# Kernel optimization log

Measured on AMD Instinct MI355X. Metric: run time of the kernel, lower is better.

Reference implementation:

```python
import jax, jax.numpy as jnp
import numpy as np

D_MODEL = 1024
NUM_HEADS = 16
DEPTH = D_MODEL // NUM_HEADS
NEG_INF = -1e9


def setup_inputs() -> dict:
    key = jax.random.key(0)
    ks = jax.random.split(key, 12)
    B, S = 4, 2048
    scale = 1.0 / np.sqrt(D_MODEL)
    inp = {
        "q": jax.random.normal(ks[0], (B, S, D_MODEL), jnp.float32),
        "k": jax.random.normal(ks[1], (B, S, D_MODEL), jnp.float32),
        "v": jax.random.normal(ks[2], (B, S, D_MODEL), jnp.float32),
        "mask": jax.random.randint(ks[3], (B, 1, 1, S), 0, 2, jnp.int32),
        "wq": jax.random.normal(ks[4], (D_MODEL, D_MODEL), jnp.float32) * scale,
        "bq": jnp.zeros((D_MODEL,), jnp.float32),
        "wk": jax.random.normal(ks[5], (D_MODEL, D_MODEL), jnp.float32) * scale,
        "bk": jnp.zeros((D_MODEL,), jnp.float32),
        "wv": jax.random.normal(ks[6], (D_MODEL, D_MODEL), jnp.float32) * scale,
        "bv": jnp.zeros((D_MODEL,), jnp.float32),
        "wo": jax.random.normal(ks[7], (D_MODEL, D_MODEL), jnp.float32) * scale,
        "bo": jnp.zeros((D_MODEL,), jnp.float32),
    }
    return inp


def _split_heads(x):
    # [B, S, D] -> [B, H, S, depth]
    B, S, _ = x.shape
    return x.reshape(B, S, NUM_HEADS, DEPTH).transpose(0, 2, 1, 3)


def reference(q, k, v, mask, wq, bq, wk, bk, wv, bv, wo, bo):
    B, S, _ = q.shape
    qh = _split_heads(q @ wq + bq)  # [B,H,S,d]
    kh = _split_heads(k @ wk + bk)
    vh = _split_heads(v @ wv + bv)
    logits = jnp.einsum("bhqd,bhkd->bhqk", qh, kh) / jnp.sqrt(
        jnp.asarray(DEPTH, jnp.float32))
    logits = logits + mask.astype(jnp.float32) * NEG_INF
    weights = jax.nn.softmax(logits, axis=-1)
    attn = jnp.einsum("bhqk,bhkd->bhqd", weights, vh)
    attn = attn.transpose(0, 2, 1, 3).reshape(B, S, D_MODEL)
    return attn @ wo + bo
```

## Files before the change

### kernel.cpp

```cpp
#include <hip/hip_runtime.h>

#define SB 4
#define SS 2048
#define SD 1024
#define SH 16

typedef float f32x4 __attribute__((ext_vector_type(4)));
typedef __bf16 bf16x8 __attribute__((ext_vector_type(8)));
typedef short short4v __attribute__((ext_vector_type(4)));
typedef unsigned int uint2v __attribute__((ext_vector_type(2)));

__device__ __forceinline__ unsigned short f2bf_(float x) {
    unsigned u = __builtin_bit_cast(unsigned, x);
    unsigned r = u + 0x7FFFu + ((u >> 16) & 1u);
    return (unsigned short)(r >> 16);
}

#define GL2LDS(g, l) __builtin_amdgcn_global_load_lds( \
    (const __attribute__((address_space(1))) unsigned int*)(g), \
    (__attribute__((address_space(3))) unsigned int*)(l), 16, 0, 0)

__global__ __launch_bounds__(256) void maskprep(
        const int* __restrict__ mk, float* __restrict__ MA, int n) {
    int i = blockIdx.x * 256 + threadIdx.x;
    if (i < n)
        MA[i] = (float)mk[i] * (-1e9f * 1.4426950408889634f) - 8.0f;
}

__global__ __launch_bounds__(256) void transpose4(
        const float* __restrict__ w0, const float* __restrict__ w1,
        const float* __restrict__ w2, const float* __restrict__ w3,
        unsigned short* __restrict__ out) {
    __shared__ unsigned short tile[32][33];
    int zz = blockIdx.z;
    const float* src = (zz == 0) ? w0 : (zz == 1) ? w1 : (zz == 2) ? w2 : w3;
    unsigned short* dst = out + (size_t)zz * 1024 * 1024;
    int x = blockIdx.x * 32 + threadIdx.x;
    int y0 = blockIdx.y * 32;
    for (int j = threadIdx.y; j < 32; j += 8)
        tile[j][threadIdx.x] = f2bf_(src[(size_t)(y0 + j) * 1024 + x]);
    __syncthreads();
    int ox = y0 + threadIdx.x;
    int oy0 = blockIdx.x * 32;
    for (int j = threadIdx.y; j < 32; j += 8)
        dst[(size_t)(oy0 + j) * 1024 + ox] = tile[threadIdx.x][j];
}

template <int STORE_MODE>
__global__ __launch_bounds__(256) void gemm_proj(
        const float* __restrict__ Af, const unsigned short* __restrict__ BT,
        const float* __restrict__ bias, unsigned short* __restrict__ C,
        float oscale) {
    const int K = 1024, N = 1024;
    __shared__ alignas(16) float Asmf[2][128][32];
    __shared__ alignas(16) unsigned short Bsm[2][128][32];
    const int m0 = blockIdx.x * 128, n0 = blockIdx.y * 128;
    const int lane = threadIdx.x & 63, wid = threadIdx.x >> 6;
    const int wr = wid >> 1, wc = wid & 1;
    const int cl = lane & 15, kg = lane >> 4;

    f32x4 acc[4][4] = {};

    auto STAGE = [&](int buf, int k0) {
#pragma unroll
        for (int i = 0; i < 4; ++i) {
            int base = i * 32 + wid * 8;
            int row = base + (lane >> 3);
            int cs = (lane & 7) ^ (row & 7);
            GL2LDS(Af + (size_t)(m0 + row) * K + k0 + cs * 4, &Asmf[buf][base][0]);
        }
#pragma unroll
        for (int i = 0; i < 2; ++i) {
            int base = (i * 4 + wid) * 16;
            int row = base + (lane >> 2);
            int cs = (lane & 3) ^ ((row >> 1) & 3);
            GL2LDS(BT + (size_t)(n0 + row) * K + k0 + cs * 8, &Bsm[buf][base][0]);
        }
    };

    STAGE(0, 0);
    __syncthreads();

    for (int k0 = 0; k0 < K; k0 += 32) {
        int cur = (k0 >> 5) & 1;
        if (k0 + 32 < K) STAGE(cur ^ 1, k0 + 32);

        bf16x8 af[4], bfv[4];
#pragma unroll
        for (int mi = 0; mi < 4; ++mi) {
            int r = wr * 64 + mi * 16 + cl;
            const float* Ar = &Asmf[cur][r][0];
            f32x4 a0 = *(const f32x4*)(Ar + ((2 * kg) ^ (r & 7)) * 4);
            f32x4 a1 = *(const f32x4*)(Ar + ((2 * kg + 1) ^ (r & 7)) * 4);
#pragma unroll
            for (int e = 0; e < 4; ++e) {
                af[mi][e] = (__bf16)a0[e];
                af[mi][4 + e] = (__bf16)a1[e];
            }
        }
#pragma unroll
        for (int ni = 0; ni < 4; ++ni) {
            int r = wc * 64 + ni * 16 + cl;
            bfv[ni] = *(const bf16x8*)&Bsm[cur][r][(kg ^ ((r >> 1) & 3)) * 8];
        }
#pragma unroll
        for (int mi = 0; mi < 4; ++mi)
#pragma unroll
            for (int ni = 0; ni < 4; ++ni)
                acc[mi][ni] = __builtin_amdgcn_mfma_f32_16x16x32_bf16(
                    af[mi], bfv[ni], acc[mi][ni], 0, 0, 0);
        __syncthreads();
    }

    const int rl = (lane >> 4) * 4;
#pragma unroll
    for (int mi = 0; mi < 4; ++mi) {
#pragma unroll
        for (int ni = 0; ni < 4; ++ni) {
            int row = m0 + wr * 64 + mi * 16 + rl;
            int col = n0 + wc * 64 + ni * 16 + cl;
            float bv = bias[col];
            f32x4 v = acc[mi][ni];
            if (STORE_MODE == 0) {
#pragma unroll
                for (int j = 0; j < 4; ++j)
                    C[(size_t)(row + j) * N + col] = f2bf_((v[j] + bv) * oscale);
            } else {
                int bb = row >> 11, s = row & 2047;
                short4v pk;
#pragma unroll
                for (int j = 0; j < 4; ++j)
                    pk[j] = (short)f2bf_(v[j] + bv);
                *(short4v*)&C[((size_t)(bb * 1024 + col)) * 2048 + s] = pk;
            }
        }
    }
}

__global__ __launch_bounds__(256) void gemm_out(
        const unsigned short* __restrict__ Ab, const unsigned short* __restrict__ BT,
        const float* __restrict__ bias, float* __restrict__ C,
        int M, int N, int K) {
    __shared__ alignas(16) unsigned short Asmb[2][128][32];
    __shared__ alignas(16) unsigned short Bsm[2][128][32];
    const int m0 = blockIdx.x * 128, n0 = blockIdx.y * 128;
    const int lane = threadIdx.x & 63, wid = threadIdx.x >> 6;
    const int wr = wid >> 1, wc = wid & 1;
    const int cl = lane & 15, kg = lane >> 4;

    f32x4 acc[4][4] = {};

    auto STAGE = [&](int buf, int k0) {
#pragma unroll
        for (int i = 0; i < 2; ++i) {
            int base = (i * 4 + wid) * 16;
            int row = base + (lane >> 2);
            int cs = (lane & 3) ^ ((row >> 1) & 3);
            GL2LDS(Ab + (size_t)(m0 + row) * K + k0 + cs * 8, &Asmb[buf][base][0]);
            GL2LDS(BT + (size_t)(n0 + row) * K + k0 + cs * 8, &Bsm[buf][base][0]);
        }
    };

    STAGE(0, 0);
    __syncthreads();

    for (int k0 = 0; k0 < K; k0 += 32) {
        int cur = (k0 >> 5) & 1;
        if (k0 + 32 < K) STAGE(cur ^ 1, k0 + 32);

        bf16x8 af[4], bfv[4];
#pragma unroll
        for (int mi = 0; mi < 4; ++mi) {
            int r = wr * 64 + mi * 16 + cl;
            af[mi] = *(const bf16x8*)&Asmb[cur][r][(kg ^ ((r >> 1) & 3)) * 8];
        }
#pragma unroll
        for (int ni = 0; ni < 4; ++ni) {
            int r = wc * 64 + ni * 16 + cl;
            bfv[ni] = *(const bf16x8*)&Bsm[cur][r][(kg ^ ((r >> 1) & 3)) * 8];
        }
#pragma unroll
        for (int mi = 0; mi < 4; ++mi)
#pragma unroll
            for (int ni = 0; ni < 4; ++ni)
                acc[mi][ni] = __builtin_amdgcn_mfma_f32_16x16x32_bf16(
                    af[mi], bfv[ni], acc[mi][ni], 0, 0, 0);
        __syncthreads();
    }

    const int rl = (lane >> 4) * 4;
#pragma unroll
    for (int mi = 0; mi < 4; ++mi) {
#pragma unroll
        for (int ni = 0; ni < 4; ++ni) {
            int row = m0 + wr * 64 + mi * 16 + rl;
            int col = n0 + wc * 64 + ni * 16 + cl;
            float bv = bias[col];
            f32x4 v = acc[mi][ni];
#pragma unroll
            for (int j = 0; j < 4; ++j)
                C[(size_t)(row + j) * N + col] = v[j] + bv;
        }
    }
}

__global__ __launch_bounds__(512, 4) void attn_kernel(
        const unsigned short* __restrict__ Qp, const unsigned short* __restrict__ Kp,
        const unsigned short* __restrict__ VT, const float* __restrict__ MA,
        unsigned short* __restrict__ O) {
    __shared__ alignas(16) unsigned short Klds[2][128][64];
    __shared__ alignas(16) unsigned short Vlds[2][64][128];
    const int lane = threadIdx.x & 63, wid = threadIdx.x >> 6;
    const int bh = blockIdx.x;
    const int b = bh >> 4, h = bh & 15;
    const int qt = blockIdx.y;
    const int qrow0 = qt * 256 + wid * 32;
    const int cl = lane & 15, kg = lane >> 4;

    bf16x8 qf[2][2];
#pragma unroll
    for (int qh = 0; qh < 2; ++qh)
#pragma unroll
        for (int kh = 0; kh < 2; ++kh)
            qf[qh][kh] = *(const bf16x8*)&Qp[(size_t)(b * SS + qrow0 + qh * 16 + cl) * SD
                                            + h * 64 + kh * 32 + kg * 8];

    const float* MAb = MA + b * SS;

    f32x4 oacc[2][4] = {};
    f32x4 lsum[2] = {};

    auto STAGE = [&](int buf, int tt) {
        int kt = (tt & 15) * 128;
        {
            int r8 = lane >> 3, c8 = lane & 7;
#pragma unroll
            for (int i = 0; i < 2; ++i) {
                int r = i * 64 + wid * 8 + r8;
                int cs = c8 ^ (r & 7);
                GL2LDS(Kp + (size_t)(b * SS + kt + r) * SD + h * 64 + cs * 8,
                       &Klds[buf][i * 64 + wid * 8][0]);
            }
        }
        {
            int r16 = lane >> 4, c16 = lane & 15;
#pragma unroll
            for (int i = 0; i < 2; ++i) {
                int r = i * 32 + wid * 4 + r16;
                int cs = (c16 & 8) | ((c16 & 7) ^ (r & 7));
                GL2LDS(VT + (size_t)(b * 1024 + h * 64 + r) * 2048 + kt + cs * 8,
                       &Vlds[buf][i * 32 + wid * 4][0]);
            }
        }
    };

    auto QKCOL = [&](int buf, int kt, int cf, f32x4* sv) {
        int r = cf * 16 + cl;
        bf16x8 kf0 = *(const bf16x8*)&Klds[buf][r][((0 + kg) ^ (r & 7)) * 8];
        bf16x8 kf1 = *(const bf16x8*)&Klds[buf][r][((4 + kg) ^ (r & 7)) * 8];
        f32x4 M = *(const f32x4*)&MAb[kt + cf * 16 + 4 * kg];
        __builtin_amdgcn_s_setprio(1);
#pragma unroll
        for (int qh = 0; qh < 2; ++qh) {
            f32x4 s = {};
            s = __builtin_amdgcn_mfma_f32_16x16x32_bf16(kf0, qf[qh][0], s, 0, 0, 0);
            s = __builtin_amdgcn_mfma_f32_16x16x32_bf16(kf1, qf[qh][1], s, 0, 0, 0);
#pragma unroll
            for (int j = 0; j < 4; ++j)
                s[j] = __builtin_amdgcn_exp2f(s[j] + M[j]);
            sv[qh] = s;
            lsum[qh] += s;
        }
        __builtin_amdgcn_s_setprio(0);
    };

    auto STEP = [&](int buf, int t) {
        int kt = t * 128;
#pragma unroll
        for (int ks = 0; ks < 4; ++ks) {
            f32x4 sA[2], sB[2];
            QKCOL(buf, kt, ks, sA);
            QKCOL(buf, kt, ks + 4, sB);
            bf16x8 pa[2];
#pragma unroll
            for (int qh = 0; qh < 2; ++qh) {
                pa[qh][0] = (__bf16)sA[qh][0];
                pa[qh][1] = (__bf16)sA[qh][1];
                pa[qh][2] = (__bf16)sA[qh][2];
                pa[qh][3] = (__bf16)sA[qh][3];
                pa[qh][4] = (__bf16)sB[qh][0];
                pa[qh][5] = (__bf16)sB[qh][1];
                pa[qh][6] = (__bf16)sB[qh][2];
                pa[qh][7] = (__bf16)sB[qh][3];
            }
            __builtin_amdgcn_s_setprio(1);
#pragma unroll
            for (int nf = 0; nf < 4; ++nf) {
                int d = nf * 16 + cl;
                int c16a = 2 * ks + (kg >> 1);
                int c16b = 2 * (ks + 4) + (kg >> 1);
                int cha = (c16a & 8) | ((c16a & 7) ^ (d & 7));
                int chb = (c16b & 8) | ((c16b & 7) ^ (d & 7));
                const char* vb = (const char*)&Vlds[buf][d][0];
                uint2v lo = *(const uint2v*)(vb + cha * 16 + (kg & 1) * 8);
                uint2v hi = *(const uint2v*)(vb + chb * 16 + (kg & 1) * 8);
                bf16x8 vf;
                *(uint2v*)&vf = lo;
                *((uint2v*)&vf + 1) = hi;
#pragma unroll
                for (int qh = 0; qh < 2; ++qh)
                    oacc[qh][nf] = __builtin_amdgcn_mfma_f32_16x16x32_bf16(
                        pa[qh], vf, oacc[qh][nf], 0, 0, 0);
            }
            __builtin_amdgcn_s_setprio(0);
        }
    };

    STAGE(0, 0);
    __syncthreads();
    for (int t = 0; t < 16; ++t) {
        int cur = t & 1;
        STAGE(cur ^ 1, t + 1);
        STEP(cur, t);
        __syncthreads();
    }

    float lfull[2];
#pragma unroll
    for (int qh = 0; qh < 2; ++qh) {
        float l = (lsum[qh][0] + lsum[qh][1]) + (lsum[qh][2] + lsum[qh][3]);
        l += __shfl_xor(l, 16);
        l += __shfl_xor(l, 32);
        lfull[qh] = l;
    }
#pragma unroll
    for (int qh = 0; qh < 2; ++qh) {
#pragma unroll
        for (int j = 0; j < 4; ++j) {
            float inv = 1.0f / __shfl(lfull[qh], 4 * kg + j);
#pragma unroll
            for (int nf = 0; nf < 4; ++nf)
                O[(size_t)(b * SS + qrow0 + qh * 16 + 4 * kg + j) * SD + h * 64 + nf * 16 + cl] =
                    f2bf_(oacc[qh][nf][j] * inv);
        }
    }
}

extern "C" void kernel_launch(void* const* d_in, const int* in_sizes, int n_in,
                              void* d_out, int out_size, void* d_ws, size_t ws_size,
                              hipStream_t stream) {
    const float* q  = (const float*)d_in[0];
    const float* k  = (const float*)d_in[1];
    const float* v  = (const float*)d_in[2];
    const int*   mk = (const int*)d_in[3];
    const float* wq = (const float*)d_in[4];
    const float* bq = (const float*)d_in[5];
    const float* wk = (const float*)d_in[6];
    const float* bk = (const float*)d_in[7];
    const float* wv = (const float*)d_in[8];
    const float* bv = (const float*)d_in[9];
    const float* wo = (const float*)d_in[10];
    const float* bo = (const float*)d_in[11];
    float* out = (float*)d_out;

    char* ws = (char*)d_ws;
    unsigned short* WT  = (unsigned short*)ws;
    unsigned short* X   = (unsigned short*)(ws + 8388608);
    unsigned short* Qh  = (unsigned short*)(ws + 25165824);
    unsigned short* Kh  = (unsigned short*)(ws + 41943040);
    unsigned short* VTr = (unsigned short*)(ws + 58720256);
    float*          MAf = (float*)(ws + 75497472);

    const float QSCL = 0.125f * 1.4426950408889634f;

    transpose4<<<dim3(32, 32, 4), dim3(32, 8), 0, stream>>>(wq, wk, wv, wo, WT);
    maskprep<<<dim3(32), dim3(256), 0, stream>>>(mk, MAf, SB * SS);

    dim3 gg(64, 8), gb(256);

    gemm_proj<0><<<gg, gb, 0, stream>>>(q, WT,               bq, Qh,  QSCL);
    gemm_proj<0><<<gg, gb, 0, stream>>>(k, WT + 1048576,     bk, Kh,  1.0f);
    gemm_proj<1><<<gg, gb, 0, stream>>>(v, WT + 2 * 1048576, bv, VTr, 1.0f);

    attn_kernel<<<dim3(64, 8), dim3(512), 0, stream>>>(Qh, Kh, VTr, MAf, X);

    gemm_out<<<dim3(64, 8), dim3(256), 0, stream>>>(
        X, WT + 3 * 1048576, bo, out, 8192, 1024, 1024);
}
```

Measured before the change: 213.7 us.

## Merge QKV projection launches and compute softmax row sums via MFMA

The three Q/K/V projection GEMM launches become one launch with a z-dimension that selects the input, weights, bias and store layout per block. This removes launch gaps and gives a larger grid of 1536 blocks for the GPU to fill. In the attention kernel, the per-lane VALU accumulation of exp values plus the final cross-lane shuffle reduction is replaced by an extra MFMA per step that multiplies the bf16 probabilities by a ones vector. That saves VALU adds and shuffles but adds matrix-core work, and the row sums now come from bf16-rounded probabilities, which keeps them consistent with the values used in P·V.

```diff
diff --git a/kernel.cpp b/kernel.cpp
--- a/kernel.cpp
+++ b/kernel.cpp
@@ -46,14 +46,21 @@
         dst[(size_t)(oy0 + j) * 1024 + ox] = tile[threadIdx.x][j];
 }
 
-template <int STORE_MODE>
-__global__ __launch_bounds__(256) void gemm_proj(
-        const float* __restrict__ Af, const unsigned short* __restrict__ BT,
-        const float* __restrict__ bias, unsigned short* __restrict__ C,
-        float oscale) {
+__global__ __launch_bounds__(256) void gemm_qkv(
+        const float* __restrict__ Aq, const float* __restrict__ Ak,
+        const float* __restrict__ Avv, const unsigned short* __restrict__ WT,
+        const float* __restrict__ bq, const float* __restrict__ bk,
+        const float* __restrict__ bv, unsigned short* __restrict__ Qh,
+        unsigned short* __restrict__ Kh, unsigned short* __restrict__ VTr,
+        float qscl) {
     const int K = 1024, N = 1024;
     __shared__ alignas(16) float Asmf[2][128][32];
     __shared__ alignas(16) unsigned short Bsm[2][128][32];
+    const int zone = blockIdx.z;
+    const float* Af = (zone == 0) ? Aq : (zone == 1) ? Ak : Avv;
+    const unsigned short* BT = WT + (size_t)zone * 1048576;
+    const float* bias = (zone == 0) ? bq : (zone == 1) ? bk : bv;
+
     const int m0 = blockIdx.x * 128, n0 = blockIdx.y * 128;
     const int lane = threadIdx.x & 63, wid = threadIdx.x >> 6;
     const int wr = wid >> 1, wc = wid & 1;
@@ -113,25 +120,27 @@
     }
 
     const int rl = (lane >> 4) * 4;
+    float os = (zone == 0) ? qscl : 1.0f;
 #pragma unroll
     for (int mi = 0; mi < 4; ++mi) {
 #pragma unroll
         for (int ni = 0; ni < 4; ++ni) {
             int row = m0 + wr * 64 + mi * 16 + rl;
             int col = n0 + wc * 64 + ni * 16 + cl;
-            float bv = bias[col];
+            float bvv = bias[col];
             f32x4 v = acc[mi][ni];
-            if (STORE_MODE == 0) {
+            if (zone < 2) {
+                unsigned short* C = (zone == 0) ? Qh : Kh;
 #pragma unroll
                 for (int j = 0; j < 4; ++j)
-                    C[(size_t)(row + j) * N + col] = f2bf_((v[j] + bv) * oscale);
+                    C[(size_t)(row + j) * N + col] = f2bf_((v[j] + bvv) * os);
             } else {
                 int bb = row >> 11, s = row & 2047;
                 short4v pk;
 #pragma unroll
                 for (int j = 0; j < 4; ++j)
-                    pk[j] = (short)f2bf_(v[j] + bv);
-                *(short4v*)&C[((size_t)(bb * 1024 + col)) * 2048 + s] = pk;
+                    pk[j] = (short)f2bf_(v[j] + bvv);
+                *(short4v*)&VTr[((size_t)(bb * 1024 + col)) * 2048 + s] = pk;
             }
         }
     }
@@ -227,8 +236,12 @@
 
     const float* MAb = MA + b * SS;
 
+    bf16x8 onesf;
+#pragma unroll
+    for (int e = 0; e < 8; ++e) onesf[e] = (__bf16)1.0f;
+
     f32x4 oacc[2][4] = {};
-    f32x4 lsum[2] = {};
+    f32x4 lacc[2] = {};
 
     auto STAGE = [&](int buf, int tt) {
         int kt = (tt & 15) * 128;
@@ -269,7 +282,6 @@
             for (int j = 0; j < 4; ++j)
                 s[j] = __builtin_amdgcn_exp2f(s[j] + M[j]);
             sv[qh] = s;
-            lsum[qh] += s;
         }
         __builtin_amdgcn_s_setprio(0);
     };
@@ -294,6 +306,10 @@
                 pa[qh][7] = (__bf16)sB[qh][3];
             }
             __builtin_amdgcn_s_setprio(1);
+#pragma unroll
+            for (int qh = 0; qh < 2; ++qh)
+                lacc[qh] = __builtin_amdgcn_mfma_f32_16x16x32_bf16(
+                    pa[qh], onesf, lacc[qh], 0, 0, 0);
 #pragma unroll
             for (int nf = 0; nf < 4; ++nf) {
                 int d = nf * 16 + cl;
@@ -325,19 +341,11 @@
         __syncthreads();
     }
 
-    float lfull[2];
 #pragma unroll
     for (int qh = 0; qh < 2; ++qh) {
-        float l = (lsum[qh][0] + lsum[qh][1]) + (lsum[qh][2] + lsum[qh][3]);
-        l += __shfl_xor(l, 16);
-        l += __shfl_xor(l, 32);
-        lfull[qh] = l;
-    }
-#pragma unroll
-    for (int qh = 0; qh < 2; ++qh) {
 #pragma unroll
         for (int j = 0; j < 4; ++j) {
-            float inv = 1.0f / __shfl(lfull[qh], 4 * kg + j);
+            float inv = 1.0f / lacc[qh][j];
 #pragma unroll
             for (int nf = 0; nf < 4; ++nf)
                 O[(size_t)(b * SS + qrow0 + qh * 16 + 4 * kg + j) * SD + h * 64 + nf * 16 + cl] =
@@ -376,11 +384,8 @@
     transpose4<<<dim3(32, 32, 4), dim3(32, 8), 0, stream>>>(wq, wk, wv, wo, WT);
     maskprep<<<dim3(32), dim3(256), 0, stream>>>(mk, MAf, SB * SS);
 
-    dim3 gg(64, 8), gb(256);
-
-    gemm_proj<0><<<gg, gb, 0, stream>>>(q, WT,               bq, Qh,  QSCL);
-    gemm_proj<0><<<gg, gb, 0, stream>>>(k, WT + 1048576,     bk, Kh,  1.0f);
-    gemm_proj<1><<<gg, gb, 0, stream>>>(v, WT + 2 * 1048576, bv, VTr, 1.0f);
+    gemm_qkv<<<dim3(64, 8, 3), dim3(256), 0, stream>>>(
+        q, k, v, WT, bq, bk, bv, Qh, Kh, VTr, QSCL);
 
     attn_kernel<<<dim3(64, 8), dim3(512), 0, stream>>>(Qh, Kh, VTr, MAf, X);
 
```

Result: faster. 206.4 us (-3.5%).
